# Kernel optimization log

Hardware: AMD Instinct MI355X
Metric: run time of the kernel (lower is better)

Reference implementation:

```python
import jax, jax.numpy as jnp
import numpy as np

N = 131072
K = 27
FIN = 3
FOUT = 32
EPS = 1e-5


def _bn(h, gamma, beta, mean, var):
    return (h - mean) * jax.lax.rsqrt(var + EPS) * gamma + beta


def setup_inputs() -> dict:
    key = jax.random.key(0)
    ks = jax.random.split(key, 8)
    return {
        "x_feats": jax.random.normal(ks[0], (N, FIN), jnp.float32),
        "z_feats": jax.random.normal(ks[1], (N, FIN), jnp.float32),
        "nbr_idx": jax.random.randint(ks[2], (N, K), 0, N, jnp.int32),
        "w1": jax.random.normal(ks[3], (K, FIN, FOUT), jnp.float32) * 0.2,
        "bn1_gamma": jnp.ones((FOUT,), jnp.float32),
        "bn1_beta": jnp.zeros((FOUT,), jnp.float32),
        "bn1_mean": jax.random.normal(ks[4], (FOUT,), jnp.float32) * 0.1,
        "bn1_var": jax.random.uniform(ks[5], (FOUT,), jnp.float32, 0.5, 1.5),
        "w2": jax.random.normal(ks[6], (K, FOUT, FOUT), jnp.float32) * 0.1,
        "mlp_w": jax.random.normal(ks[7], (FIN, FOUT), jnp.float32) * 0.3,
        "mlp_b": jnp.zeros((FOUT,), jnp.float32),
        "mlp_gamma": jnp.ones((FOUT,), jnp.float32),
        "mlp_beta": jnp.zeros((FOUT,), jnp.float32),
        "mlp_mean": jnp.zeros((FOUT,), jnp.float32),
        "mlp_var": jnp.ones((FOUT,), jnp.float32),
    }


def reference(x_feats, z_feats, nbr_idx, w1, bn1_gamma, bn1_beta, bn1_mean,
              bn1_var, w2, mlp_w, mlp_b, mlp_gamma, mlp_beta, mlp_mean,
              mlp_var):
    # --- voxel branch: sparse conv (gather-GEMM) -> BN -> SiLU -> sparse conv
    g1 = x_feats[nbr_idx]                       # [N, K, FIN] irregular gather
    h = jnp.einsum('nkf,kfo->no', g1, w1)       # [N, FOUT]
    h = jax.nn.silu(_bn(h, bn1_gamma, bn1_beta, bn1_mean, bn1_var))
    g2 = h[nbr_idx]                             # [N, K, FOUT] irregular gather
    x_out = jnp.einsum('nkf,kfo->no', g2, w2)   # [N, FOUT]

    # --- point branch: SharedMLP = Linear -> BN -> ReLU
    z = z_feats @ mlp_w + mlp_b
    z = jax.nn.relu(_bn(z, mlp_gamma, mlp_beta, mlp_mean, mlp_var))

    # --- mixed_mix: fuse voxel and point features additively
    fused = x_out + z
    return (fused, fused)
```

## Files before the change

### kernel.cpp

```cpp
#include <hip/hip_runtime.h>
#include <math.h>

#define NN 131072
#define KK 27
#define FIN 3
#define FOUT 32
#define EPS 1e-5f

typedef _Float16 f16;
typedef __attribute__((ext_vector_type(8))) _Float16 f16x8;
typedef __attribute__((ext_vector_type(16))) float f32x16;

__global__ __launch_bounds__(256) void pack_w2_kernel(
    const float* __restrict__ w2, f16* __restrict__ w2p)
{
    const int t = blockIdx.x * 256 + threadIdx.x;
    if (t >= KK * 2 * 64 * 8) return;
    const int k    = t >> 10;
    const int rem  = t & 1023;
    const int half = rem >> 9;
    const int l    = (rem >> 3) & 63;
    const int j    = rem & 7;
    const int krow = half * 16 + ((l >> 5) << 3) + j;
    const int n    = l & 31;
    w2p[t] = (f16)w2[k * (FOUT * FOUT) + krow * FOUT + n];
}

__global__ __launch_bounds__(256) void conv1_kernel(
    const float* __restrict__ x_feats,
    const int*   __restrict__ nbr_idx,
    const float* __restrict__ w1,
    const float* __restrict__ g1,  const float* __restrict__ b1,
    const float* __restrict__ m1,  const float* __restrict__ v1,
    f16* __restrict__ h_out)
{
    const int n = blockIdx.x * 256 + threadIdx.x;

    int idxs[KK];
    const int* nb = nbr_idx + (size_t)n * KK;
#pragma unroll
    for (int k = 0; k < KK; ++k) idxs[k] = nb[k];

    float acc[FOUT];
#pragma unroll
    for (int o = 0; o < FOUT; ++o) acc[o] = 0.f;

#pragma unroll
    for (int c = 0; c < 3; ++c) {
        float xs[9][3];
#pragma unroll
        for (int q = 0; q < 9; ++q) {
            const float* xr = x_feats + (size_t)idxs[c * 9 + q] * FIN;
            xs[q][0] = xr[0]; xs[q][1] = xr[1]; xs[q][2] = xr[2];
        }
#pragma unroll
        for (int q = 0; q < 9; ++q) {
            const float* w = w1 + (c * 9 + q) * (FIN * FOUT);
#pragma unroll
            for (int o = 0; o < FOUT; ++o) {
                float a = acc[o];
                a = fmaf(xs[q][0], w[o],            a);
                a = fmaf(xs[q][1], w[FOUT + o],     a);
                a = fmaf(xs[q][2], w[2 * FOUT + o], a);
                acc[o] = a;
            }
        }
    }

    f16* hr = h_out + (size_t)n * FOUT;
#pragma unroll
    for (int g = 0; g < 4; ++g) {
        f16x8 hv;
#pragma unroll
        for (int j = 0; j < 8; ++j) {
            const int o = g * 8 + j;
            const float sc = g1[o] * rsqrtf(v1[o] + EPS);
            float v = (acc[o] - m1[o]) * sc + b1[o];
            v = v / (1.f + __expf(-v));
            hv[j] = (f16)v;
        }
        *(f16x8*)(hr + g * 8) = hv;
    }
}

__global__ __launch_bounds__(256) void conv2_mfma_kernel(
    const f16*   __restrict__ h,
    const int*   __restrict__ nbr_idx,
    const f16*   __restrict__ w2p,
    const float* __restrict__ z_feats,
    const float* __restrict__ mlp_w,
    const float* __restrict__ mlp_b,
    const float* __restrict__ mg, const float* __restrict__ mbe,
    const float* __restrict__ mm, const float* __restrict__ mv,
    float* __restrict__ out)
{
    const int lane = threadIdx.x & 63;
    const int wave = threadIdx.x >> 6;
    const int base = (blockIdx.x * 4 + wave) * 32;
    const int row  = lane & 31;
    const int hi   = lane >> 5;

    int idxs[KK];
    const int* nb = nbr_idx + (size_t)(base + row) * KK;
#pragma unroll
    for (int k = 0; k < KK; ++k) idxs[k] = nb[k];

    f32x16 acc0 = {};
    f32x16 acc1 = {};

    const f16x8* bp = (const f16x8*)w2p;

    const f16* hr0 = h + (size_t)idxs[0] * FOUT + hi * 8;
    f16x8 a1 = *(const f16x8*)hr0;
    f16x8 a2 = *(const f16x8*)(hr0 + 16);
    f16x8 b1 = bp[lane];
    f16x8 b2 = bp[64 + lane];

#pragma unroll
    for (int k = 0; k < KK; ++k) {
        f16x8 na1, na2, nb1, nb2;
        if (k + 1 < KK) {
            const f16* hr = h + (size_t)idxs[k + 1] * FOUT + hi * 8;
            na1 = *(const f16x8*)hr;
            na2 = *(const f16x8*)(hr + 16);
            nb1 = bp[(k + 1) * 128 + lane];
            nb2 = bp[(k + 1) * 128 + 64 + lane];
        }
        __builtin_amdgcn_s_setprio(1);
        acc0 = __builtin_amdgcn_mfma_f32_32x32x16_f16(a1, b1, acc0, 0, 0, 0);
        acc1 = __builtin_amdgcn_mfma_f32_32x32x16_f16(a2, b2, acc1, 0, 0, 0);
        __builtin_amdgcn_s_setprio(0);
        a1 = na1; a2 = na2; b1 = nb1; b2 = nb2;
    }

    const int n0 = lane & 31;
    const float wc0 = mlp_w[n0];
    const float wc1 = mlp_w[FOUT + n0];
    const float wc2 = mlp_w[2 * FOUT + n0];
    const float sc  = mg[n0] * rsqrtf(mv[n0] + EPS);
    const float bi  = mlp_b[n0];
    const float mmv = mm[n0];
    const float mbv = mbe[n0];

#pragma unroll
    for (int r = 0; r < 16; ++r) {
        const int m    = (r & 3) + ((r >> 2) << 3) + (hi << 2);
        const int node = base + m;
        const float* zr = z_feats + (size_t)node * FIN;
        float z = bi;
        z = fmaf(zr[0], wc0, z);
        z = fmaf(zr[1], wc1, z);
        z = fmaf(zr[2], wc2, z);
        z = (z - mmv) * sc + mbv;
        z = fmaxf(z, 0.f);
        const float v = acc0[r] + acc1[r] + z;
        out[(size_t)node * FOUT + n0] = v;
        out[(size_t)NN * FOUT + (size_t)node * FOUT + n0] = v;
    }
}

extern "C" void kernel_launch(void* const* d_in, const int* in_sizes, int n_in,
                              void* d_out, int out_size, void* d_ws, size_t ws_size,
                              hipStream_t stream) {
    const float* x_feats = (const float*)d_in[0];
    const float* z_feats = (const float*)d_in[1];
    const int*   nbr_idx = (const int*)d_in[2];
    const float* w1      = (const float*)d_in[3];
    const float* bn1_g   = (const float*)d_in[4];
    const float* bn1_b   = (const float*)d_in[5];
    const float* bn1_m   = (const float*)d_in[6];
    const float* bn1_v   = (const float*)d_in[7];
    const float* w2      = (const float*)d_in[8];
    const float* mlp_w   = (const float*)d_in[9];
    const float* mlp_b   = (const float*)d_in[10];
    const float* mlp_g   = (const float*)d_in[11];
    const float* mlp_be  = (const float*)d_in[12];
    const float* mlp_m   = (const float*)d_in[13];
    const float* mlp_v   = (const float*)d_in[14];

    f16* h   = (f16*)d_ws;
    f16* w2p = (f16*)((char*)d_ws + (size_t)8 * 1024 * 1024);
    float* out = (float*)d_out;

    pack_w2_kernel<<<(KK * 1024 + 255) / 256, 256, 0, stream>>>(w2, w2p);
    conv1_kernel<<<NN / 256, 256, 0, stream>>>(x_feats, nbr_idx, w1,
                                               bn1_g, bn1_b, bn1_m, bn1_v, h);
    conv2_mfma_kernel<<<NN / 128, 256, 0, stream>>>(h, nbr_idx, w2p, z_feats,
                                                    mlp_w, mlp_b, mlp_g, mlp_be,
                                                    mlp_m, mlp_v, out);
}
```

Baseline: 173.5 us.

## Deepen conv2 gather prefetch to six stages and fold w2 packing into conv1

The conv2 MFMA loop now keeps six neighbour steps of h and w2p loads in flight, issued through inline-asm global loads with explicit vmcnt waits, where it previously prefetched only one step ahead. This is meant to hide the latency of the irregular gather. The separate pack_w2 launch is merged into the conv1 kernel as 27 extra blocks, which removes one kernel launch. The cost is more VGPRs for the 24 staged vectors, which may lower occupancy, and fragile hand-written waitcnt logic.

```diff
diff --git a/kernel.cpp b/kernel.cpp
--- a/kernel.cpp
+++ b/kernel.cpp
@@ -9,31 +9,37 @@
 
 typedef _Float16 f16;
 typedef __attribute__((ext_vector_type(8))) _Float16 f16x8;
-typedef __attribute__((ext_vector_type(16))) float f32x16;
-
-__global__ __launch_bounds__(256) void pack_w2_kernel(
-    const float* __restrict__ w2, f16* __restrict__ w2p)
+typedef __attribute__((ext_vector_type(4)))  float   f32x4;
+typedef __attribute__((ext_vector_type(16))) float   f32x16;
+
+__device__ __forceinline__ void pack_w2_block(
+    const float* __restrict__ w2, f16* __restrict__ w2p, int k, int t)
 {
-    const int t = blockIdx.x * 256 + threadIdx.x;
-    if (t >= KK * 2 * 64 * 8) return;
-    const int k    = t >> 10;
-    const int rem  = t & 1023;
-    const int half = rem >> 9;
-    const int l    = (rem >> 3) & 63;
-    const int j    = rem & 7;
-    const int krow = half * 16 + ((l >> 5) << 3) + j;
-    const int n    = l & 31;
-    w2p[t] = (f16)w2[k * (FOUT * FOUT) + krow * FOUT + n];
-}
-
-__global__ __launch_bounds__(256) void conv1_kernel(
+#pragma unroll
+    for (int r = 0; r < 4; ++r) {
+        const int e    = r * 256 + t;
+        const int half = e >> 9;
+        const int l    = (e >> 3) & 63;
+        const int j    = e & 7;
+        const int krow = half * 16 + ((l >> 5) << 3) + j;
+        const int n    = l & 31;
+        w2p[k * 1024 + e] = (f16)w2[k * (FOUT * FOUT) + krow * FOUT + n];
+    }
+}
+
+__global__ __launch_bounds__(256) void conv1_pack_kernel(
     const float* __restrict__ x_feats,
     const int*   __restrict__ nbr_idx,
     const float* __restrict__ w1,
     const float* __restrict__ g1,  const float* __restrict__ b1,
     const float* __restrict__ m1,  const float* __restrict__ v1,
-    f16* __restrict__ h_out)
+    f16* __restrict__ h_out,
+    const float* __restrict__ w2, f16* __restrict__ w2p)
 {
+    if (blockIdx.x >= NN / 256) {
+        pack_w2_block(w2, w2p, blockIdx.x - NN / 256, threadIdx.x);
+        return;
+    }
     const int n = blockIdx.x * 256 + threadIdx.x;
 
     int idxs[KK];
@@ -104,34 +110,54 @@
     const int* nb = nbr_idx + (size_t)(base + row) * KK;
 #pragma unroll
     for (int k = 0; k < KK; ++k) idxs[k] = nb[k];
+#pragma unroll
+    for (int k = 0; k < KK; ++k) asm volatile("" : "+v"(idxs[k]));
 
     f32x16 acc0 = {};
     f32x16 acc1 = {};
 
-    const f16x8* bp = (const f16x8*)w2p;
-
-    const f16* hr0 = h + (size_t)idxs[0] * FOUT + hi * 8;
-    f16x8 a1 = *(const f16x8*)hr0;
-    f16x8 a2 = *(const f16x8*)(hr0 + 16);
-    f16x8 b1 = bp[lane];
-    f16x8 b2 = bp[64 + lane];
+    f32x4 wa1[6], wa2[6], wb1[6], wb2[6];
+
+#define C2_ISSUE(t, s) do {                                                  \
+        const f16* hr_ = h + (size_t)idxs[t] * FOUT + hi * 8;                \
+        const f16* bb_ = w2p + (t) * 1024 + lane * 8;                        \
+        asm volatile("global_load_dwordx4 %0, %1, off"                       \
+                     : "=v"(wa1[s]) : "v"(hr_));                             \
+        asm volatile("global_load_dwordx4 %0, %1, off"                       \
+                     : "=v"(wa2[s]) : "v"(hr_ + 16));                        \
+        asm volatile("global_load_dwordx4 %0, %1, off"                       \
+                     : "=v"(wb1[s]) : "v"(bb_));                             \
+        asm volatile("global_load_dwordx4 %0, %1, off"                       \
+                     : "=v"(wb2[s]) : "v"(bb_ + 512));                       \
+    } while (0)
+
+#pragma unroll
+    for (int t = 0; t < 6; ++t) C2_ISSUE(t, t);
 
 #pragma unroll
     for (int k = 0; k < KK; ++k) {
-        f16x8 na1, na2, nb1, nb2;
-        if (k + 1 < KK) {
-            const f16* hr = h + (size_t)idxs[k + 1] * FOUT + hi * 8;
-            na1 = *(const f16x8*)hr;
-            na2 = *(const f16x8*)(hr + 16);
-            nb1 = bp[(k + 1) * 128 + lane];
-            nb2 = bp[(k + 1) * 128 + 64 + lane];
-        }
+        const int rem = KK - 1 - k;
+        if      (rem >= 5) asm volatile("s_waitcnt vmcnt(20)");
+        else if (rem == 4) asm volatile("s_waitcnt vmcnt(16)");
+        else if (rem == 3) asm volatile("s_waitcnt vmcnt(12)");
+        else if (rem == 2) asm volatile("s_waitcnt vmcnt(8)");
+        else if (rem == 1) asm volatile("s_waitcnt vmcnt(4)");
+        else               asm volatile("s_waitcnt vmcnt(0)");
+        __builtin_amdgcn_sched_barrier(0);
+
+        const int s = k % 6;
+        const f16x8 a1 = __builtin_bit_cast(f16x8, wa1[s]);
+        const f16x8 a2 = __builtin_bit_cast(f16x8, wa2[s]);
+        const f16x8 b1 = __builtin_bit_cast(f16x8, wb1[s]);
+        const f16x8 b2 = __builtin_bit_cast(f16x8, wb2[s]);
         __builtin_amdgcn_s_setprio(1);
         acc0 = __builtin_amdgcn_mfma_f32_32x32x16_f16(a1, b1, acc0, 0, 0, 0);
         acc1 = __builtin_amdgcn_mfma_f32_32x32x16_f16(a2, b2, acc1, 0, 0, 0);
         __builtin_amdgcn_s_setprio(0);
-        a1 = na1; a2 = na2; b1 = nb1; b2 = nb2;
-    }
+
+        if (k + 6 < KK) C2_ISSUE(k + 6, s);
+    }
+#undef C2_ISSUE
 
     const int n0 = lane & 31;
     const float wc0 = mlp_w[n0];
@@ -182,10 +208,9 @@
     f16* w2p = (f16*)((char*)d_ws + (size_t)8 * 1024 * 1024);
     float* out = (float*)d_out;
 
-    pack_w2_kernel<<<(KK * 1024 + 255) / 256, 256, 0, stream>>>(w2, w2p);
-    conv1_kernel<<<NN / 256, 256, 0, stream>>>(x_feats, nbr_idx, w1,
-                                               bn1_g, bn1_b, bn1_m, bn1_v, h);
-    conv2_mfma_kernel<<<NN / 128, 256, 0, stream>>>(h, nbr_idx, w2p, z_feats,
-                                                    mlp_w, mlp_b, mlp_g, mlp_be,
-                                                    mlp_m, mlp_v, out);
-}
+    conv1_pack_kernel<<<NN / 256 + KK, 256, 0, stream>>>(
+        x_feats, nbr_idx, w1, bn1_g, bn1_b, bn1_m, bn1_v, h, w2, w2p);
+    conv2_mfma_kernel<<<NN / 128, 256, 0, stream>>>(
+        h, nbr_idx, w2p, z_feats, mlp_w, mlp_b, mlp_g, mlp_be,
+        mlp_m, mlp_v, out);
+}
```

Measured after the change: 169.1 us. 2.5% less time.
